# Performance work log

Measured on AMD Instinct MI355X. Metric: run time of the kernel, lower is better.

The kernel has to match this reference:

```python
import jax, jax.numpy as jnp
import numpy as np

B, M, E, H, A = 32, 512, 256, 8, 64


def setup_inputs() -> dict:
    key = jax.random.key(0)
    k0, k1, k2, k3, k4 = jax.random.split(key, 5)
    s = 1.0 / np.sqrt(E)
    x = jax.random.normal(k0, (B, M, E), dtype=jnp.float32)
    Wq = jax.random.normal(k1, (E, H * A), dtype=jnp.float32) * s
    Wk = jax.random.normal(k2, (E, H * A), dtype=jnp.float32) * s
    Wv = jax.random.normal(k3, (E, H * A), dtype=jnp.float32) * s
    Wr = jax.random.normal(k4, (E, A), dtype=jnp.float32) * s
    return {"x": x, "Wq": Wq, "Wk": Wk, "Wv": Wv, "Wr": Wr}


def reference(x, Wq, Wk, Wv, Wr):
    # Faithful to the original: (B, M, H*A) tensors are view()'d directly to
    # (H, B, M, A) / (H, B, A, M) without any transpose — this mixes batch
    # into the head axis exactly as the torch code does.
    q = (x @ Wq).reshape(H, B, M, A)   # query view
    k = (x @ Wk).reshape(H, B, A, M)   # keys viewed pre-transposed
    v = (x @ Wv).reshape(H, B, M, A)
    scores = jnp.einsum('hbma,hban->hbmn', q, k)      # (H, B, M, M)
    att = jax.nn.softmax(scores, axis=-1)
    out = jnp.einsum('hbmn,hbna->hbma', att, v)       # (H, B, M, A)
    out = out.mean(axis=0)                            # head-mean -> (B, M, A)
    return jax.nn.relu(out + x @ Wr)
```

## Files before the change

### kernel.cpp

```cpp
#include <hip/hip_runtime.h>
#include <math.h>


typedef _Float16 f16;
typedef _Float16 f16x2 __attribute__((ext_vector_type(2)));
typedef _Float16 f16x4 __attribute__((ext_vector_type(4)));
typedef _Float16 f16x8 __attribute__((ext_vector_type(8)));
typedef float    f32x4 __attribute__((ext_vector_type(4)));

__global__ __launch_bounds__(256) void k_cast(const float* __restrict__ in,
                                              f16* __restrict__ out, int n4) {
  int i = blockIdx.x * 256 + threadIdx.x;
  if (i < n4) {
    f32x4 v = reinterpret_cast<const f32x4*>(in)[i];
    f16x4 h;
    h[0] = (f16)v[0]; h[1] = (f16)v[1]; h[2] = (f16)v[2]; h[3] = (f16)v[3];
    reinterpret_cast<f16x4*>(out)[i] = h;
  }
}

__global__ __launch_bounds__(256) void k_transpose_w(const float* __restrict__ Wq,
                                                     const float* __restrict__ Wk,
                                                     const float* __restrict__ Wv,
                                                     const float* __restrict__ Wr,
                                                     f16* __restrict__ Wt,
                                                     f16* __restrict__ Wrt) {
  __shared__ f16 tile[64][68];
  int b = blockIdx.x;
  const float* src; f16* dst; int r0, c0, Cin;
  if (b < 96) {
    int ws = b >> 5, rem = b & 31;
    src = (ws == 0) ? Wq : (ws == 1) ? Wk : Wv;
    dst = Wt + ws * 512 * 256;
    Cin = 512; r0 = (rem >> 3) * 64; c0 = (rem & 7) * 64;
  } else {
    src = Wr; dst = Wrt; Cin = 64; r0 = (b - 96) * 64; c0 = 0;
  }
  int t = threadIdx.x;
#pragma unroll
  for (int u = 0; u < 8; ++u) {
    int e = u * 256 + t;
    int r = e >> 5, c = (e & 31) << 1;
    const float* p = src + (long)(r0 + r) * Cin + (c0 + c);
    f16x2 v; v[0] = (f16)p[0]; v[1] = (f16)p[1];
    *reinterpret_cast<f16x2*>(&tile[r][c]) = v;
  }
  __syncthreads();
#pragma unroll
  for (int u = 0; u < 16; ++u) {
    int f = u * 256 + t;
    int cc = f >> 6, rr = f & 63;
    dst[(long)(c0 + cc) * 256 + (r0 + rr)] = tile[rr][cc];
  }
}

__global__ __launch_bounds__(256) void k_transpose(const f16* __restrict__ in,
                                                   f16* __restrict__ out,
                                                   int R_, int C_) {
  __shared__ f16 tile[64][68];
  int g = blockIdx.x;
  long gb = (long)g * R_ * C_;
  int r0 = blockIdx.y * 64, c0 = blockIdx.z * 64;
  int t = threadIdx.x;
#pragma unroll
  for (int u = 0; u < 8; ++u) {
    int e = u * 256 + t;
    int r = e >> 5, c = (e & 31) << 1;
    const f16* p = in + gb + (long)(r0 + r) * C_ + (c0 + c);
    f16x2 v; v[0] = p[0]; v[1] = p[1];
    *reinterpret_cast<f16x2*>(&tile[r][c]) = v;
  }
  __syncthreads();
#pragma unroll
  for (int u = 0; u < 16; ++u) {
    int f = u * 256 + t;
    int cc = f >> 6, rr = f & 63;
    out[gb + (long)(c0 + cc) * R_ + (r0 + rr)] = tile[rr][cc];
  }
}

template <int BN, bool F32OUT>
__global__ __launch_bounds__(256, 2) void k_gemm(const f16* __restrict__ Xh,
                                                 const f16* __restrict__ Wt,
                                                 f16* __restrict__ outH,
                                                 float* __restrict__ outF, int N) {
  __shared__ f16 Ash[128][72];
  __shared__ f16 Bsh[BN][72];
  constexpr int NT = BN / 32;
  int t = threadIdx.x;
  int w = t >> 6, l = t & 63;
  int lrow = l & 15, lg = l >> 4, lk8 = lg * 8;
  int wm = w >> 1, wn = w & 1;
  int rb = blockIdx.x * 128, cb = blockIdx.y * BN;

  f32x4 acc[4][NT] = {};

  for (int kt = 0; kt < 4; ++kt) {
    __syncthreads();
    int kb = kt * 64;
#pragma unroll
    for (int s = 0; s < 4; ++s) {
      int row = s * 32 + (t >> 3), k0 = (t & 7) * 8;
      *reinterpret_cast<f16x8*>(&Ash[row][k0]) =
          *reinterpret_cast<const f16x8*>(Xh + (long)(rb + row) * 256 + kb + k0);
    }
#pragma unroll
    for (int s = 0; s < BN / 32; ++s) {
      int row = s * 32 + (t >> 3), k0 = (t & 7) * 8;
      *reinterpret_cast<f16x8*>(&Bsh[row][k0]) =
          *reinterpret_cast<const f16x8*>(Wt + (long)(cb + row) * 256 + kb + k0);
    }
    __syncthreads();

    f16x8 af[4][2];
#pragma unroll
    for (int mi = 0; mi < 4; ++mi)
#pragma unroll
      for (int ks = 0; ks < 2; ++ks)
        af[mi][ks] = *reinterpret_cast<const f16x8*>(&Ash[64 * wm + 16 * mi + lrow][32 * ks + lk8]);
#pragma unroll
    for (int nt = 0; nt < NT; ++nt) {
      f16x8 b0 = *reinterpret_cast<const f16x8*>(&Bsh[(BN / 2) * wn + 16 * nt + lrow][lk8]);
      f16x8 b1 = *reinterpret_cast<const f16x8*>(&Bsh[(BN / 2) * wn + 16 * nt + lrow][32 + lk8]);
#pragma unroll
      for (int mi = 0; mi < 4; ++mi) {
        acc[mi][nt] = __builtin_amdgcn_mfma_f32_16x16x32_f16(af[mi][0], b0, acc[mi][nt], 0, 0, 0);
        acc[mi][nt] = __builtin_amdgcn_mfma_f32_16x16x32_f16(af[mi][1], b1, acc[mi][nt], 0, 0, 0);
      }
    }
  }
#pragma unroll
  for (int mi = 0; mi < 4; ++mi)
#pragma unroll
    for (int nt = 0; nt < NT; ++nt)
#pragma unroll
      for (int r = 0; r < 4; ++r) {
        int row = rb + 64 * wm + 16 * mi + 4 * lg + r;
        int col = cb + (BN / 2) * wn + 16 * nt + lrow;
        float v = acc[mi][nt][r];
        if constexpr (F32OUT) {
          outF[(long)row * N + col] = v;
        } else {
          long idx = ((long)(col >> 9) << 23) + (long)row * 512 + (col & 511);
          outH[idx] = (f16)v;
        }
      }
}

__global__ __launch_bounds__(256, 4) void k_attn(const f16* __restrict__ Qh,
                                                 const f16* __restrict__ Ktg,
                                                 const f16* __restrict__ Vtg,
                                                 f16* __restrict__ Of) {
  __shared__ f16 Ksh[64][72];
  __shared__ f16 Vsh[64][72];
  __shared__ f16 Psh[4][32][72];
  int g = blockIdx.x, mb = blockIdx.y;
  int t = threadIdx.x, w = t >> 6, l = t & 63;
  int lrow = l & 15, lg = l >> 4, lk8 = lg * 8;
  long gp = (long)g * 32768;
  const f16* Qg = Qh + gp;
  const f16* Kg = Ktg + gp;
  const f16* Vg = Vtg + gp;
  f16* Og = Of + gp;
  int m0 = mb * 128 + w * 32;

  f16x8 qf[2][2];
#pragma unroll
  for (int mi = 0; mi < 2; ++mi)
#pragma unroll
    for (int ks = 0; ks < 2; ++ks)
      qf[mi][ks] = *reinterpret_cast<const f16x8*>(Qg + (long)(m0 + 16 * mi + lrow) * 64 + 32 * ks + lk8);

  f32x4 accO[2][4] = {};
  float Mx[2] = {-INFINITY, -INFINITY}, Ls[2] = {0.f, 0.f};

  for (int c = 0; c < 8; ++c) {
    __syncthreads();
#pragma unroll
    for (int s = 0; s < 2; ++s) {
      int row = s * 32 + (t >> 3), o8 = (t & 7) * 8;
      *reinterpret_cast<f16x8*>(&Ksh[row][o8]) =
          *reinterpret_cast<const f16x8*>(Kg + (long)(c * 64 + row) * 64 + o8);
      *reinterpret_cast<f16x8*>(&Vsh[row][o8]) =
          *reinterpret_cast<const f16x8*>(Vg + (long)row * 512 + c * 64 + o8);
    }
    __syncthreads();

    f32x4 St[2][4] = {};
#pragma unroll
    for (int nt = 0; nt < 4; ++nt) {
      f16x8 k0 = *reinterpret_cast<const f16x8*>(&Ksh[16 * nt + lrow][lk8]);
      f16x8 k1 = *reinterpret_cast<const f16x8*>(&Ksh[16 * nt + lrow][32 + lk8]);
#pragma unroll
      for (int mi = 0; mi < 2; ++mi) {
        St[mi][nt] = __builtin_amdgcn_mfma_f32_16x16x32_f16(k0, qf[mi][0], St[mi][nt], 0, 0, 0);
        St[mi][nt] = __builtin_amdgcn_mfma_f32_16x16x32_f16(k1, qf[mi][1], St[mi][nt], 0, 0, 0);
      }
    }

    float scb[2][4];
#pragma unroll
    for (int mi = 0; mi < 2; ++mi) {
      float tm = St[mi][0][0];
#pragma unroll
      for (int nt = 0; nt < 4; ++nt)
#pragma unroll
        for (int r = 0; r < 4; ++r) tm = fmaxf(tm, St[mi][nt][r]);
      tm = fmaxf(tm, __shfl_xor(tm, 16));
      tm = fmaxf(tm, __shfl_xor(tm, 32));
      float nm = fmaxf(Mx[mi], tm);
      float sc = __expf(Mx[mi] - nm);
      Mx[mi] = nm;
      float ps = 0.f;
#pragma unroll
      for (int nt = 0; nt < 4; ++nt)
#pragma unroll
        for (int r = 0; r < 4; ++r) {
          float p = __expf(St[mi][nt][r] - nm);
          St[mi][nt][r] = p;
          ps += p;
        }
      ps += __shfl_xor(ps, 16);
      ps += __shfl_xor(ps, 32);
      Ls[mi] = Ls[mi] * sc + ps;
#pragma unroll
      for (int nt = 0; nt < 4; ++nt) {
        f16x4 p4;
        p4[0] = (f16)St[mi][nt][0]; p4[1] = (f16)St[mi][nt][1];
        p4[2] = (f16)St[mi][nt][2]; p4[3] = (f16)St[mi][nt][3];
        *reinterpret_cast<f16x4*>(&Psh[w][16 * mi + lrow][16 * nt + 4 * lg]) = p4;
      }
#pragma unroll
      for (int r = 0; r < 4; ++r) scb[mi][r] = __shfl(sc, 20 * lg + r);
    }
#pragma unroll
    for (int mi = 0; mi < 2; ++mi)
#pragma unroll
      for (int at = 0; at < 4; ++at)
#pragma unroll
        for (int r = 0; r < 4; ++r) accO[mi][at][r] *= scb[mi][r];

#pragma unroll
    for (int ks = 0; ks < 2; ++ks) {
      f16x8 pa[2];
#pragma unroll
      for (int mi = 0; mi < 2; ++mi)
        pa[mi] = *reinterpret_cast<const f16x8*>(&Psh[w][16 * mi + lrow][32 * ks + lk8]);
#pragma unroll
      for (int at = 0; at < 4; ++at) {
        f16x8 vb = *reinterpret_cast<const f16x8*>(&Vsh[16 * at + lrow][32 * ks + lk8]);
#pragma unroll
        for (int mi = 0; mi < 2; ++mi)
          accO[mi][at] = __builtin_amdgcn_mfma_f32_16x16x32_f16(pa[mi], vb, accO[mi][at], 0, 0, 0);
      }
    }
  }

#pragma unroll
  for (int mi = 0; mi < 2; ++mi) {
    float inv = 1.f / Ls[mi];
    float invb[4];
#pragma unroll
    for (int r = 0; r < 4; ++r) invb[r] = __shfl(inv, 20 * lg + r);
#pragma unroll
    for (int r = 0; r < 4; ++r) {
      int row = m0 + 16 * mi + 4 * lg + r;
#pragma unroll
      for (int at = 0; at < 4; ++at)
        Og[(long)row * 64 + 16 * at + lrow] = (f16)(accO[mi][at][r] * invb[r]);
    }
  }
}

__global__ __launch_bounds__(256) void k_finalize(const f16* __restrict__ Of,
                                                  const float* __restrict__ Rf,
                                                  float* __restrict__ out) {
  int i = blockIdx.x * 256 + threadIdx.x;
  f32x4 s = {};
#pragma unroll
  for (int h = 0; h < 8; ++h) {
    f16x4 o = reinterpret_cast<const f16x4*>(Of + (long)h * 1048576)[i];
#pragma unroll
    for (int j = 0; j < 4; ++j) s[j] += (float)o[j];
  }
  f32x4 r = reinterpret_cast<const f32x4*>(Rf)[i];
  f32x4 v = s * 0.125f + r;
#pragma unroll
  for (int j = 0; j < 4; ++j) v[j] = v[j] > 0.f ? v[j] : 0.f;
  reinterpret_cast<f32x4*>(out)[i] = v;
}

extern "C" void kernel_launch(void* const* d_in, const int* in_sizes, int n_in,
                              void* d_out, int out_size, void* d_ws, size_t ws_size,
                              hipStream_t stream) {
  const float* x  = (const float*)d_in[0];
  const float* Wq = (const float*)d_in[1];
  const float* Wk = (const float*)d_in[2];
  const float* Wv = (const float*)d_in[3];
  const float* Wr = (const float*)d_in[4];
  float* out = (float*)d_out;
  char* w = (char*)d_ws;

  f16*   Xh  = (f16*)(w + 0);
  f16*   Wt  = (f16*)(w + 8388608);
  f16*   Wrt = (f16*)(w + 9175040);
  f16*   Qh  = (f16*)(w + 9207808);
  f16*   Kn  = (f16*)(w + 25985024);
  f16*   Vn  = (f16*)(w + 42762240);
  f16*   Ktg = (f16*)(w + 59539456);
  f16*   Vtg = (f16*)(w + 76316672);
  float* Rf  = (float*)(w + 93093888);
  f16*   Of  = (f16*)(w + 25985024);

  k_cast<<<4096, 256, 0, stream>>>(x, Xh, 1048576);
  k_transpose_w<<<100, 256, 0, stream>>>(Wq, Wk, Wv, Wr, Wt, Wrt);

  k_gemm<128, false><<<dim3(128, 12), 256, 0, stream>>>(Xh, Wt, Qh, nullptr, 1536);
  k_gemm<64, true><<<dim3(128, 1), 256, 0, stream>>>(Xh, Wrt, nullptr, Rf, 64);

  k_transpose<<<dim3(256, 1, 8), 256, 0, stream>>>(Kn, Ktg, 64, 512);
  k_transpose<<<dim3(256, 8, 1), 256, 0, stream>>>(Vn, Vtg, 512, 64);

  k_attn<<<dim3(256, 4), 256, 0, stream>>>(Qh, Ktg, Vtg, Of);
  k_finalize<<<1024, 256, 0, stream>>>(Of, Rf, out);
}
```

Measured before the change: 153.3 us.

## Fold K/V transposes into attention staging, swizzle LDS, use direct global-to-LDS loads

Removes the two standalone K and V transpose kernels. The attention kernel now reads K and V in their natural layout and transposes them while writing into an XOR-swizzled shared-memory tile. It also prefetches the next K/V chunk into registers while the current chunk is computed. The GEMM now loads tiles with global_load_lds straight into swizzled unpadded LDS and raises the occupancy hint to 3 blocks per SU. The trade-off is scalar, scattered LDS stores for the transposed writes in attention and more register pressure from the prefetch.

```diff
diff --git a/kernel.cpp b/kernel.cpp
--- a/kernel.cpp
+++ b/kernel.cpp
@@ -7,6 +7,13 @@
 typedef _Float16 f16x4 __attribute__((ext_vector_type(4)));
 typedef _Float16 f16x8 __attribute__((ext_vector_type(8)));
 typedef float    f32x4 __attribute__((ext_vector_type(4)));
+
+typedef __attribute__((address_space(1))) const void* gas_t;
+typedef __attribute__((address_space(3))) void* las_t;
+
+__device__ __forceinline__ void gload16(const void* g, void* l) {
+  __builtin_amdgcn_global_load_lds((gas_t)g, (las_t)l, 16, 0, 0);
+}
 
 __global__ __launch_bounds__(256) void k_cast(const float* __restrict__ in,
                                               f16* __restrict__ out, int n4) {
@@ -54,61 +61,38 @@
   }
 }
 
-__global__ __launch_bounds__(256) void k_transpose(const f16* __restrict__ in,
-                                                   f16* __restrict__ out,
-                                                   int R_, int C_) {
-  __shared__ f16 tile[64][68];
-  int g = blockIdx.x;
-  long gb = (long)g * R_ * C_;
-  int r0 = blockIdx.y * 64, c0 = blockIdx.z * 64;
-  int t = threadIdx.x;
-#pragma unroll
-  for (int u = 0; u < 8; ++u) {
-    int e = u * 256 + t;
-    int r = e >> 5, c = (e & 31) << 1;
-    const f16* p = in + gb + (long)(r0 + r) * C_ + (c0 + c);
-    f16x2 v; v[0] = p[0]; v[1] = p[1];
-    *reinterpret_cast<f16x2*>(&tile[r][c]) = v;
-  }
-  __syncthreads();
-#pragma unroll
-  for (int u = 0; u < 16; ++u) {
-    int f = u * 256 + t;
-    int cc = f >> 6, rr = f & 63;
-    out[gb + (long)(c0 + cc) * R_ + (r0 + rr)] = tile[rr][cc];
-  }
-}
-
 template <int BN, bool F32OUT>
-__global__ __launch_bounds__(256, 2) void k_gemm(const f16* __restrict__ Xh,
+__global__ __launch_bounds__(256, 3) void k_gemm(const f16* __restrict__ Xh,
                                                  const f16* __restrict__ Wt,
                                                  f16* __restrict__ outH,
                                                  float* __restrict__ outF, int N) {
-  __shared__ f16 Ash[128][72];
-  __shared__ f16 Bsh[BN][72];
+  __shared__ f16 Ash[128 * 64];
+  __shared__ f16 Bsh[BN * 64];
   constexpr int NT = BN / 32;
   int t = threadIdx.x;
   int w = t >> 6, l = t & 63;
-  int lrow = l & 15, lg = l >> 4, lk8 = lg * 8;
+  int lrow = l & 15, lg = l >> 4;
   int wm = w >> 1, wn = w & 1;
   int rb = blockIdx.x * 128, cb = blockIdx.y * BN;
 
   f32x4 acc[4][NT] = {};
 
   for (int kt = 0; kt < 4; ++kt) {
+    int kb = kt * 64;
     __syncthreads();
-    int kb = kt * 64;
-#pragma unroll
-    for (int s = 0; s < 4; ++s) {
-      int row = s * 32 + (t >> 3), k0 = (t & 7) * 8;
-      *reinterpret_cast<f16x8*>(&Ash[row][k0]) =
-          *reinterpret_cast<const f16x8*>(Xh + (long)(rb + row) * 256 + kb + k0);
-    }
-#pragma unroll
-    for (int s = 0; s < BN / 32; ++s) {
-      int row = s * 32 + (t >> 3), k0 = (t & 7) * 8;
-      *reinterpret_cast<f16x8*>(&Bsh[row][k0]) =
-          *reinterpret_cast<const f16x8*>(Wt + (long)(cb + row) * 256 + kb + k0);
+#pragma unroll
+    for (int i = 0; i < 4; ++i) {
+      int slot = i * 256 + t;
+      int row = slot >> 3, pblk = slot & 7;
+      int blk = pblk ^ (row & 7);
+      gload16(Xh + (long)(rb + row) * 256 + kb + blk * 8, Ash + slot * 8);
+    }
+#pragma unroll
+    for (int i = 0; i < BN / 32; ++i) {
+      int slot = i * 256 + t;
+      int row = slot >> 3, pblk = slot & 7;
+      int blk = pblk ^ (row & 7);
+      gload16(Wt + (long)(cb + row) * 256 + kb + blk * 8, Bsh + slot * 8);
     }
     __syncthreads();
 
@@ -116,12 +100,16 @@
 #pragma unroll
     for (int mi = 0; mi < 4; ++mi)
 #pragma unroll
-      for (int ks = 0; ks < 2; ++ks)
-        af[mi][ks] = *reinterpret_cast<const f16x8*>(&Ash[64 * wm + 16 * mi + lrow][32 * ks + lk8]);
+      for (int ks = 0; ks < 2; ++ks) {
+        int r = 64 * wm + 16 * mi + lrow;
+        af[mi][ks] = *reinterpret_cast<const f16x8*>(
+            Ash + r * 64 + (((4 * ks + lg) ^ (lrow & 7)) * 8));
+      }
 #pragma unroll
     for (int nt = 0; nt < NT; ++nt) {
-      f16x8 b0 = *reinterpret_cast<const f16x8*>(&Bsh[(BN / 2) * wn + 16 * nt + lrow][lk8]);
-      f16x8 b1 = *reinterpret_cast<const f16x8*>(&Bsh[(BN / 2) * wn + 16 * nt + lrow][32 + lk8]);
+      int rB = (BN / 2) * wn + 16 * nt + lrow;
+      f16x8 b0 = *reinterpret_cast<const f16x8*>(Bsh + rB * 64 + ((lg ^ (lrow & 7)) * 8));
+      f16x8 b1 = *reinterpret_cast<const f16x8*>(Bsh + rB * 64 + (((4 + lg) ^ (lrow & 7)) * 8));
 #pragma unroll
       for (int mi = 0; mi < 4; ++mi) {
         acc[mi][nt] = __builtin_amdgcn_mfma_f32_16x16x32_f16(af[mi][0], b0, acc[mi][nt], 0, 0, 0);
@@ -135,7 +123,7 @@
     for (int nt = 0; nt < NT; ++nt)
 #pragma unroll
       for (int r = 0; r < 4; ++r) {
-        int row = rb + 64 * wm + 16 * mi + 4 * lg + r;
+        int row = rb + 64 * wm + 16 * mi + 4 * (l >> 4) + r;
         int col = cb + (BN / 2) * wn + 16 * nt + lrow;
         float v = acc[mi][nt][r];
         if constexpr (F32OUT) {
@@ -148,22 +136,25 @@
 }
 
 __global__ __launch_bounds__(256, 4) void k_attn(const f16* __restrict__ Qh,
-                                                 const f16* __restrict__ Ktg,
-                                                 const f16* __restrict__ Vtg,
+                                                 const f16* __restrict__ Kn,
+                                                 const f16* __restrict__ Vn,
                                                  f16* __restrict__ Of) {
-  __shared__ f16 Ksh[64][72];
-  __shared__ f16 Vsh[64][72];
+  __shared__ f16 Ksh[64 * 64];
+  __shared__ f16 Vsh[64 * 64];
   __shared__ f16 Psh[4][32][72];
   int g = blockIdx.x, mb = blockIdx.y;
   int t = threadIdx.x, w = t >> 6, l = t & 63;
   int lrow = l & 15, lg = l >> 4, lk8 = lg * 8;
   long gp = (long)g * 32768;
   const f16* Qg = Qh + gp;
-  const f16* Kg = Ktg + gp;
-  const f16* Vg = Vtg + gp;
+  const f16* Kg = Kn + gp;
+  const f16* Vg = Vn + gp;
   f16* Og = Of + gp;
   int m0 = mb * 128 + w * 32;
 
+  int sa = t >> 3;
+  int so = (t & 7) * 8;
+
   f16x8 qf[2][2];
 #pragma unroll
   for (int mi = 0; mi < 2; ++mi)
@@ -174,27 +165,57 @@
   f32x4 accO[2][4] = {};
   float Mx[2] = {-INFINITY, -INFINITY}, Ls[2] = {0.f, 0.f};
 
+  auto write_stage = [&](f16x8 kr0, f16x8 kr1, f16x8 vr0, f16x8 vr1) {
+#pragma unroll
+    for (int s = 0; s < 2; ++s) {
+      f16x8 kr = s ? kr1 : kr0;
+      int a = s * 32 + sa;
+      int ab = a >> 3;
+#pragma unroll
+      for (int j = 0; j < 8; ++j) {
+        int n = so + j;
+        Ksh[n * 64 + ((ab ^ (n >> 3)) * 8) + (a & 7)] = kr[j];
+      }
+      f16x8 vr = s ? vr1 : vr0;
+      int n2 = s * 32 + sa;
+      int nb = n2 >> 3;
+#pragma unroll
+      for (int j = 0; j < 8; ++j) {
+        int aa = so + j;
+        Vsh[aa * 64 + ((nb ^ (aa >> 3)) * 8) + (n2 & 7)] = vr[j];
+      }
+    }
+  };
+
+  {
+    f16x8 k0 = *reinterpret_cast<const f16x8*>(Kg + (long)(0 * 32 + sa) * 512 + so);
+    f16x8 k1 = *reinterpret_cast<const f16x8*>(Kg + (long)(1 * 32 + sa) * 512 + so);
+    f16x8 v0 = *reinterpret_cast<const f16x8*>(Vg + (long)(0 * 32 + sa) * 64 + so);
+    f16x8 v1 = *reinterpret_cast<const f16x8*>(Vg + (long)(32 + sa) * 64 + so);
+    write_stage(k0, k1, v0, v1);
+  }
+  __syncthreads();
+
   for (int c = 0; c < 8; ++c) {
-    __syncthreads();
-#pragma unroll
-    for (int s = 0; s < 2; ++s) {
-      int row = s * 32 + (t >> 3), o8 = (t & 7) * 8;
-      *reinterpret_cast<f16x8*>(&Ksh[row][o8]) =
-          *reinterpret_cast<const f16x8*>(Kg + (long)(c * 64 + row) * 64 + o8);
-      *reinterpret_cast<f16x8*>(&Vsh[row][o8]) =
-          *reinterpret_cast<const f16x8*>(Vg + (long)row * 512 + c * 64 + o8);
-    }
-    __syncthreads();
+    f16x8 kn0, kn1, vn0, vn1;
+    if (c < 7) {
+      int cn = c + 1;
+      kn0 = *reinterpret_cast<const f16x8*>(Kg + (long)(0 * 32 + sa) * 512 + cn * 64 + so);
+      kn1 = *reinterpret_cast<const f16x8*>(Kg + (long)(1 * 32 + sa) * 512 + cn * 64 + so);
+      vn0 = *reinterpret_cast<const f16x8*>(Vg + (long)(cn * 64 + sa) * 64 + so);
+      vn1 = *reinterpret_cast<const f16x8*>(Vg + (long)(cn * 64 + 32 + sa) * 64 + so);
+    }
 
     f32x4 St[2][4] = {};
 #pragma unroll
     for (int nt = 0; nt < 4; ++nt) {
-      f16x8 k0 = *reinterpret_cast<const f16x8*>(&Ksh[16 * nt + lrow][lk8]);
-      f16x8 k1 = *reinterpret_cast<const f16x8*>(&Ksh[16 * nt + lrow][32 + lk8]);
+      int n = 16 * nt + lrow, nb = n >> 3;
+      f16x8 ka = *reinterpret_cast<const f16x8*>(Ksh + n * 64 + ((lg ^ nb) * 8));
+      f16x8 kb = *reinterpret_cast<const f16x8*>(Ksh + n * 64 + (((4 + lg) ^ nb) * 8));
 #pragma unroll
       for (int mi = 0; mi < 2; ++mi) {
-        St[mi][nt] = __builtin_amdgcn_mfma_f32_16x16x32_f16(k0, qf[mi][0], St[mi][nt], 0, 0, 0);
-        St[mi][nt] = __builtin_amdgcn_mfma_f32_16x16x32_f16(k1, qf[mi][1], St[mi][nt], 0, 0, 0);
+        St[mi][nt] = __builtin_amdgcn_mfma_f32_16x16x32_f16(ka, qf[mi][0], St[mi][nt], 0, 0, 0);
+        St[mi][nt] = __builtin_amdgcn_mfma_f32_16x16x32_f16(kb, qf[mi][1], St[mi][nt], 0, 0, 0);
       }
     }
 
@@ -248,12 +269,17 @@
         pa[mi] = *reinterpret_cast<const f16x8*>(&Psh[w][16 * mi + lrow][32 * ks + lk8]);
 #pragma unroll
       for (int at = 0; at < 4; ++at) {
-        f16x8 vb = *reinterpret_cast<const f16x8*>(&Vsh[16 * at + lrow][32 * ks + lk8]);
+        int a = 16 * at + lrow, ab = a >> 3;
+        f16x8 vb = *reinterpret_cast<const f16x8*>(Vsh + a * 64 + (((4 * ks + lg) ^ ab) * 8));
 #pragma unroll
         for (int mi = 0; mi < 2; ++mi)
           accO[mi][at] = __builtin_amdgcn_mfma_f32_16x16x32_f16(pa[mi], vb, accO[mi][at], 0, 0, 0);
       }
     }
+
+    __syncthreads();
+    if (c < 7) write_stage(kn0, kn1, vn0, vn1);
+    __syncthreads();
   }
 
 #pragma unroll
@@ -301,26 +327,22 @@
   float* out = (float*)d_out;
   char* w = (char*)d_ws;
 
-  f16*   Xh  = (f16*)(w + 0);
-  f16*   Wt  = (f16*)(w + 8388608);
-  f16*   Wrt = (f16*)(w + 9175040);
-  f16*   Qh  = (f16*)(w + 9207808);
-  f16*   Kn  = (f16*)(w + 25985024);
-  f16*   Vn  = (f16*)(w + 42762240);
-  f16*   Ktg = (f16*)(w + 59539456);
-  f16*   Vtg = (f16*)(w + 76316672);
-  float* Rf  = (float*)(w + 93093888);
-  f16*   Of  = (f16*)(w + 25985024);
+  f16*   Xh   = (f16*)(w + 0);
+  f16*   Wt   = (f16*)(w + 8388608);
+  f16*   Wrt  = (f16*)(w + 9175040);
+  f16*   QKV  = (f16*)(w + 9207808);
+  f16*   Qh   = QKV;
+  f16*   Kn   = (f16*)(w + 25985024);
+  f16*   Vn   = (f16*)(w + 42762240);
+  float* Rf   = (float*)(w + 59539456);
+  f16*   Of   = (f16*)(w + 63733760);
 
   k_cast<<<4096, 256, 0, stream>>>(x, Xh, 1048576);
   k_transpose_w<<<100, 256, 0, stream>>>(Wq, Wk, Wv, Wr, Wt, Wrt);
 
-  k_gemm<128, false><<<dim3(128, 12), 256, 0, stream>>>(Xh, Wt, Qh, nullptr, 1536);
+  k_gemm<128, false><<<dim3(128, 12), 256, 0, stream>>>(Xh, Wt, QKV, nullptr, 512);
   k_gemm<64, true><<<dim3(128, 1), 256, 0, stream>>>(Xh, Wrt, nullptr, Rf, 64);
 
-  k_transpose<<<dim3(256, 1, 8), 256, 0, stream>>>(Kn, Ktg, 64, 512);
-  k_transpose<<<dim3(256, 8, 1), 256, 0, stream>>>(Vn, Vtg, 512, 64);
-
-  k_attn<<<dim3(256, 4), 256, 0, stream>>>(Qh, Ktg, Vtg, Of);
+  k_attn<<<dim3(256, 4), 256, 0, stream>>>(Qh, Kn, Vn, Of);
   k_finalize<<<1024, 256, 0, stream>>>(Of, Rf, out);
 }
```

After: 155.1 us. About the same (+1.2%).
